# Kernel tuning notes

Measured on AMD Instinct MI355X. Metric: run time of the kernel, lower is better.

The kernel has to match this reference:

```python
import jax, jax.numpy as jnp
import numpy as np

B, N, E, F, H = 4, 10000, 320000, 128, 128


def setup_inputs() -> dict:
    key = jax.random.key(0)
    ks = jax.random.split(key, 12)
    s = 1.0 / np.sqrt(F)
    sh = 1.0 / np.sqrt(H)
    return {
        "batch_feat": jax.random.normal(ks[0], (B, N, F), dtype=jnp.float32),
        "batch_edges": jax.random.randint(ks[1], (B, 2, E), 0, N, dtype=jnp.int32),
        "batch_attr": jax.random.uniform(ks[2], (B, E), dtype=jnp.float32),
        "W1": jax.random.uniform(ks[3], (F, H), jnp.float32, -s, s),
        "b1": jnp.zeros((H,), jnp.float32),
        "W2": jax.random.uniform(ks[4], (H, H), jnp.float32, -sh, sh),
        "b2": jnp.zeros((H,), jnp.float32),
        "W3": jax.random.uniform(ks[5], (H, H), jnp.float32, -sh, sh),
        "b3": jnp.zeros((H,), jnp.float32),
        "Wl": jax.random.uniform(ks[6], (H, 1), jnp.float32, -sh, sh),
        "bl": jnp.zeros((1,), jnp.float32),
    }


def reference(batch_feat, batch_edges, batch_attr, W1, b1, W2, b2, W3, b3, Wl, bl):
    n_nodes = batch_feat.shape[1]

    def gcn_conv(x, row, col, w, W, b):
        # PyG gcn_norm with add_self_loops=False: deg = scatter_add(w, col)
        deg = jax.ops.segment_sum(w, col, num_segments=n_nodes)  # [N]
        dinv = jnp.where(deg > 0, jax.lax.rsqrt(deg), 0.0)
        norm = dinv[row] * w * dinv[col]                         # [E]
        xw = x @ W                                               # [N,H]
        msg = norm[:, None] * xw[row]                            # gather [E,H]
        return jax.ops.segment_sum(msg, col, num_segments=n_nodes) + b

    def per_graph(x, ei, w):
        row, col = ei[0], ei[1]
        h = jax.nn.relu(gcn_conv(x, row, col, w, W1, b1))
        h = jax.nn.relu(gcn_conv(h, row, col, w, W2, b2))
        h = jax.nn.relu(gcn_conv(h, row, col, w, W3, b3))
        return h.mean(axis=0) @ Wl + bl                          # [1]

    return jax.vmap(per_graph)(batch_feat, batch_edges, batch_attr)  # [B,1]
```

## Files before the change

### kernel.cpp

```cpp
#include <hip/hip_runtime.h>

#define BB 4
#define NN 10000
#define EE 320000
#define HH 128
#define HALFN 5000
#define NK2 (2 * NN)
#define RS (2 * NN + 1)

__global__ __launch_bounds__(256) void rank_kernel(
    const int* __restrict__ edges, int* __restrict__ cnt, int* __restrict__ rank) {
  int b = blockIdx.y;
  int e0 = (blockIdx.x * 256 + threadIdx.x) * 2;
  int2 rr = *(const int2*)(edges + (size_t)b * 2 * EE + e0);
  int2 cc = *(const int2*)(edges + (size_t)b * 2 * EE + EE + e0);
  int k0 = ((rr.x >= HALFN) ? NN : 0) + cc.x;
  int k1 = ((rr.y >= HALFN) ? NN : 0) + cc.y;
  int r0 = atomicAdd(&cnt[b * NK2 + k0], 1);
  int r1 = atomicAdd(&cnt[b * NK2 + k1], 1);
  *(int2*)(rank + (size_t)b * EE + e0) = make_int2(r0, r1);
}

__global__ __launch_bounds__(256) void scan_kernel(
    const int* __restrict__ cnt, int* __restrict__ rowstart) {
  int b = blockIdx.x, t = threadIdx.x;
  __shared__ int s[256];
  int running = 0;
  for (int base = 0; base < NK2; base += 2048) {
    int v[8];
    int i0 = base + t * 8;
    int tsum = 0;
#pragma unroll
    for (int j = 0; j < 8; ++j) {
      v[j] = (i0 + j < NK2) ? cnt[b * NK2 + i0 + j] : 0;
      tsum += v[j];
    }
    s[t] = tsum;
    __syncthreads();
    for (int o = 1; o < 256; o <<= 1) {
      int add = (t >= o) ? s[t - o] : 0;
      __syncthreads();
      s[t] += add;
      __syncthreads();
    }
    int ex = running + s[t] - tsum;
#pragma unroll
    for (int j = 0; j < 8; ++j) {
      if (i0 + j < NK2) rowstart[b * RS + i0 + j] = ex;
      ex += v[j];
    }
    int tot = s[255];
    __syncthreads();
    running += tot;
  }
  if (t == 0) rowstart[b * RS + NK2] = running;
}

__global__ __launch_bounds__(256) void fill_kernel(
    const int* __restrict__ edges, const float* __restrict__ attr,
    const int* __restrict__ rank, const int* __restrict__ rowstart,
    int2* __restrict__ csr) {
  int b = blockIdx.y;
  int e0 = (blockIdx.x * 256 + threadIdx.x) * 2;
  int2 rr = *(const int2*)(edges + (size_t)b * 2 * EE + e0);
  int2 cc = *(const int2*)(edges + (size_t)b * 2 * EE + EE + e0);
  float2 ww = *(const float2*)(attr + (size_t)b * EE + e0);
  int2 rk = *(const int2*)(rank + (size_t)b * EE + e0);
  int k0 = ((rr.x >= HALFN) ? NN : 0) + cc.x;
  int k1 = ((rr.y >= HALFN) ? NN : 0) + cc.y;
  int p0 = rowstart[b * RS + k0] + rk.x;
  int p1 = rowstart[b * RS + k1] + rk.y;
  csr[(size_t)b * EE + p0] = make_int2(rr.x, __float_as_int(ww.x));
  csr[(size_t)b * EE + p1] = make_int2(rr.y, __float_as_int(ww.y));
}

__global__ __launch_bounds__(256) void deg_kernel(
    const int2* __restrict__ csr, const int* __restrict__ rowstart,
    float* __restrict__ dinv) {
  int b = blockIdx.y;
  int n = blockIdx.x * 256 + threadIdx.x;
  if (n >= NN) return;
  const int2* c = csr + (size_t)b * EE;
  float sum = 0.f;
#pragma unroll
  for (int q = 0; q < 2; ++q) {
    int key = q * NN + n;
    int s0 = rowstart[b * RS + key], s1 = rowstart[b * RS + key + 1];
    for (int i = s0; i < s1; ++i) sum += __int_as_float(c[i].y);
  }
  dinv[b * NN + n] = sum > 0.f ? rsqrtf(sum) : 0.f;
}

__global__ __launch_bounds__(256) void gemm_kernel(
    const float* __restrict__ x, const float* __restrict__ W,
    float* __restrict__ out) {
  __shared__ float xs[32 * 68];
  __shared__ float ws[32 * 144];
  int b = blockIdx.y;
  int row0 = blockIdx.x * 64;
  int t = threadIdx.x;
  int rg = t >> 4, cg = t & 15;
  int fc = cg * 8 + ((cg >> 2) << 2);
  float acc[4][8];
#pragma unroll
  for (int r = 0; r < 4; ++r)
#pragma unroll
    for (int j = 0; j < 8; ++j) acc[r][j] = 0.f;
  const float* xb = x + (size_t)b * NN * HH;

  for (int k0 = 0; k0 < HH; k0 += 32) {
#pragma unroll
    for (int i = 0; i < 2; ++i) {
      int idx = t + i * 256;
      int rl = idx >> 3, kq = idx & 7;
      int row = row0 + rl;
      float4 v = make_float4(0.f, 0.f, 0.f, 0.f);
      if (row < NN) v = *(const float4*)(xb + (size_t)row * HH + k0 + kq * 4);
      xs[(kq * 4 + 0) * 68 + rl] = v.x;
      xs[(kq * 4 + 1) * 68 + rl] = v.y;
      xs[(kq * 4 + 2) * 68 + rl] = v.z;
      xs[(kq * 4 + 3) * 68 + rl] = v.w;
    }
#pragma unroll
    for (int i = 0; i < 4; ++i) {
      int idx = t + i * 256;
      int kk = idx >> 5, c = (idx & 31) * 4;
      float4 v = *(const float4*)(W + (size_t)(k0 + kk) * HH + c);
      int f = c + ((c >> 5) << 2);
      *(float4*)&ws[kk * 144 + f] = v;
    }
    __syncthreads();
#pragma unroll 4
    for (int k = 0; k < 32; ++k) {
      float4 xv = *(const float4*)&xs[k * 68 + rg * 4];
      float4 w0 = *(const float4*)&ws[k * 144 + fc];
      float4 w1 = *(const float4*)&ws[k * 144 + fc + 4];
      const float* xp = (const float*)&xv;
#pragma unroll
      for (int r = 0; r < 4; ++r) {
        acc[r][0] += xp[r] * w0.x; acc[r][1] += xp[r] * w0.y;
        acc[r][2] += xp[r] * w0.z; acc[r][3] += xp[r] * w0.w;
        acc[r][4] += xp[r] * w1.x; acc[r][5] += xp[r] * w1.y;
        acc[r][6] += xp[r] * w1.z; acc[r][7] += xp[r] * w1.w;
      }
    }
    __syncthreads();
  }
#pragma unroll
  for (int r = 0; r < 4; ++r) {
    int row = row0 + rg * 4 + r;
    if (row < NN) {
      float* og = out + ((size_t)b * NN + row) * HH + cg * 8;
      *(float4*)og = make_float4(acc[r][0], acc[r][1], acc[r][2], acc[r][3]);
      *(float4*)(og + 4) = make_float4(acc[r][4], acc[r][5], acc[r][6], acc[r][7]);
    }
  }
}

__global__ __launch_bounds__(256) void agg_kernel(
    const float* __restrict__ xw, const int2* __restrict__ csr,
    const int* __restrict__ rowstart, const float* __restrict__ dinv,
    const float* __restrict__ bias, float* __restrict__ h, int phase) {
  int g = blockIdx.x & 7;
  int b = g >> 1;
  int q = g & 1;
  int chunk = blockIdx.x >> 3;
  int nhalf = (phase == 0) ? q : 1 - q;
  int half = (threadIdx.x >> 5) & 1;
  int n = nhalf * HALFN + chunk * 8 + (threadIdx.x >> 6) * 2 + half;
  int sl = threadIdx.x & 31;
  int key = q * NN + n;
  int s0 = rowstart[b * RS + key], s1 = rowstart[b * RS + key + 1];
  const float* xwg = xw + (size_t)b * NN * HH;
  const float* dv = dinv + b * NN;
  const int2* c = csr + (size_t)b * EE;
  float4 a0 = make_float4(0.f, 0.f, 0.f, 0.f);
  float4 a1 = make_float4(0.f, 0.f, 0.f, 0.f);
  float4 a2 = make_float4(0.f, 0.f, 0.f, 0.f);
  float4 a3 = make_float4(0.f, 0.f, 0.f, 0.f);
  int i = s0;
  for (; i + 4 <= s1; i += 4) {
    int2 e0 = c[i];
    int2 e1 = c[i + 1];
    int2 e2 = c[i + 2];
    int2 e3 = c[i + 3];
    float w0 = __int_as_float(e0.y) * dv[e0.x];
    float w1 = __int_as_float(e1.y) * dv[e1.x];
    float w2 = __int_as_float(e2.y) * dv[e2.x];
    float w3 = __int_as_float(e3.y) * dv[e3.x];
    float4 v0 = *(const float4*)(xwg + (size_t)e0.x * HH + sl * 4);
    float4 v1 = *(const float4*)(xwg + (size_t)e1.x * HH + sl * 4);
    float4 v2 = *(const float4*)(xwg + (size_t)e2.x * HH + sl * 4);
    float4 v3 = *(const float4*)(xwg + (size_t)e3.x * HH + sl * 4);
    a0.x += w0 * v0.x; a0.y += w0 * v0.y; a0.z += w0 * v0.z; a0.w += w0 * v0.w;
    a1.x += w1 * v1.x; a1.y += w1 * v1.y; a1.z += w1 * v1.z; a1.w += w1 * v1.w;
    a2.x += w2 * v2.x; a2.y += w2 * v2.y; a2.z += w2 * v2.z; a2.w += w2 * v2.w;
    a3.x += w3 * v3.x; a3.y += w3 * v3.y; a3.z += w3 * v3.z; a3.w += w3 * v3.w;
  }
  for (; i < s1; ++i) {
    int2 e0 = c[i];
    float w0 = __int_as_float(e0.y) * dv[e0.x];
    float4 v0 = *(const float4*)(xwg + (size_t)e0.x * HH + sl * 4);
    a0.x += w0 * v0.x; a0.y += w0 * v0.y; a0.z += w0 * v0.z; a0.w += w0 * v0.w;
  }
  a0.x += a1.x + a2.x + a3.x;
  a0.y += a1.y + a2.y + a3.y;
  a0.z += a1.z + a2.z + a3.z;
  a0.w += a1.w + a2.w + a3.w;
  float* hp = h + ((size_t)b * NN + n) * HH + sl * 4;
  if (phase == 0) {
    *(float4*)hp = a0;
  } else {
    float dn = dv[n];
    float4 prev = *(const float4*)hp;
    float4 bb = *(const float4*)(bias + sl * 4);
    *(float4*)hp = make_float4(fmaxf((prev.x + a0.x) * dn + bb.x, 0.f),
                               fmaxf((prev.y + a0.y) * dn + bb.y, 0.f),
                               fmaxf((prev.z + a0.z) * dn + bb.z, 0.f),
                               fmaxf((prev.w + a0.w) * dn + bb.w, 0.f));
  }
}

__global__ __launch_bounds__(64) void init_out_kernel(float* out, const float* __restrict__ bl) {
  if (threadIdx.x < BB) out[threadIdx.x] = bl[0];
}

__global__ __launch_bounds__(256) void final_kernel(
    const float* __restrict__ h, const float* __restrict__ Wl,
    float* __restrict__ out) {
  int b = blockIdx.y;
  int t = threadIdx.x;
  int f = t & 127;
  int rr = t >> 7;
  float p = 0.f;
  for (int n = blockIdx.x * 2 + rr; n < NN; n += gridDim.x * 2)
    p += h[((size_t)b * NN + n) * HH + f];
  __shared__ float s[256];
  s[t] = p;
  __syncthreads();
  float v = 0.f;
  if (t < 128) v = (s[t] + s[t + 128]) * Wl[f];
  __syncthreads();
  s[t] = v;
  __syncthreads();
  for (int o = 64; o > 0; o >>= 1) {
    if (t < o) s[t] += s[t + o];
    __syncthreads();
  }
  if (t == 0) atomicAdd(&out[b], s[0] * (1.0f / NN));
}

extern "C" void kernel_launch(void* const* d_in, const int* in_sizes, int n_in,
                              void* d_out, int out_size, void* d_ws, size_t ws_size,
                              hipStream_t stream) {
  const float* feat = (const float*)d_in[0];
  const int* edges = (const int*)d_in[1];
  const float* attr = (const float*)d_in[2];
  const float* W1 = (const float*)d_in[3];
  const float* b1 = (const float*)d_in[4];
  const float* W2 = (const float*)d_in[5];
  const float* b2 = (const float*)d_in[6];
  const float* W3 = (const float*)d_in[7];
  const float* b3 = (const float*)d_in[8];
  const float* Wl = (const float*)d_in[9];
  const float* bl = (const float*)d_in[10];
  float* out = (float*)d_out;

  char* ws = (char*)d_ws;
  size_t off = 0;
  auto alloc = [&](size_t bytes) {
    size_t o = off;
    off = (off + bytes + 255) & ~(size_t)255;
    return o;
  };
  int*   cnt      = (int*)  (ws + alloc((size_t)BB * NK2 * 4));
  int*   rowstart = (int*)  (ws + alloc((size_t)BB * RS * 4));
  int2*  csr      = (int2*) (ws + alloc((size_t)BB * EE * 8));
  float* xw       = (float*)(ws + alloc((size_t)BB * NN * HH * 4));
  float* h        = (float*)(ws + alloc((size_t)BB * NN * HH * 4));
  int*   rank = (int*)xw;
  float* dinv = (float*)cnt;

  (void)hipMemsetAsync(cnt, 0, (size_t)BB * NK2 * 4, stream);

  dim3 egrid2(EE / 512, BB);
  rank_kernel<<<egrid2, 256, 0, stream>>>(edges, cnt, rank);
  scan_kernel<<<BB, 256, 0, stream>>>(cnt, rowstart);
  fill_kernel<<<egrid2, 256, 0, stream>>>(edges, attr, rank, rowstart, csr);
  deg_kernel<<<dim3((NN + 255) / 256, BB), 256, 0, stream>>>(csr, rowstart, dinv);

  dim3 ggrid((NN + 63) / 64, BB);
  int agrid = 8 * (HALFN / 8);

  gemm_kernel<<<ggrid, 256, 0, stream>>>(feat, W1, xw);
  agg_kernel<<<agrid, 256, 0, stream>>>(xw, csr, rowstart, dinv, b1, h, 0);
  agg_kernel<<<agrid, 256, 0, stream>>>(xw, csr, rowstart, dinv, b1, h, 1);
  gemm_kernel<<<ggrid, 256, 0, stream>>>(h, W2, xw);
  agg_kernel<<<agrid, 256, 0, stream>>>(xw, csr, rowstart, dinv, b2, h, 0);
  agg_kernel<<<agrid, 256, 0, stream>>>(xw, csr, rowstart, dinv, b2, h, 1);
  gemm_kernel<<<ggrid, 256, 0, stream>>>(h, W3, xw);
  agg_kernel<<<agrid, 256, 0, stream>>>(xw, csr, rowstart, dinv, b3, h, 0);
  agg_kernel<<<agrid, 256, 0, stream>>>(xw, csr, rowstart, dinv, b3, h, 1);

  init_out_kernel<<<1, 64, 0, stream>>>(out, bl);
  final_kernel<<<dim3(64, BB), 256, 0, stream>>>(h, Wl, out);
}
```

Measured before the change: 381.9 us.

## Replace global atomic ranking with per-block LDS histograms and column scan

Swaps the global-atomic counting sort used to build the CSR for a two-level scheme. Each of 64 blocks per graph builds a shared-memory histogram of destination columns, one half of the row split at a time, and records 16-bit local ranks. A column-scan kernel then turns the per-block histograms into block offsets and totals, and the fill kernel adds the global rowstart, the block offset and the local rank. This removes heavily contended global atomics, but adds a 64x20000 histogram buffer written and scanned per graph, an extra launch, and blocks that run only 256 threads with a 40 KB LDS array.

Result: faster. 373.3 us (-2.2%).

```diff
diff --git a/kernel.cpp b/kernel.cpp
--- a/kernel.cpp
+++ b/kernel.cpp
@@ -7,18 +7,51 @@
 #define HALFN 5000
 #define NK2 (2 * NN)
 #define RS (2 * NN + 1)
-
-__global__ __launch_bounds__(256) void rank_kernel(
-    const int* __restrict__ edges, int* __restrict__ cnt, int* __restrict__ rank) {
-  int b = blockIdx.y;
-  int e0 = (blockIdx.x * 256 + threadIdx.x) * 2;
-  int2 rr = *(const int2*)(edges + (size_t)b * 2 * EE + e0);
-  int2 cc = *(const int2*)(edges + (size_t)b * 2 * EE + EE + e0);
-  int k0 = ((rr.x >= HALFN) ? NN : 0) + cc.x;
-  int k1 = ((rr.y >= HALFN) ? NN : 0) + cc.y;
-  int r0 = atomicAdd(&cnt[b * NK2 + k0], 1);
-  int r1 = atomicAdd(&cnt[b * NK2 + k1], 1);
-  *(int2*)(rank + (size_t)b * EE + e0) = make_int2(r0, r1);
+#define NHB 64
+#define EPB (EE / NHB)
+
+__global__ __launch_bounds__(256) void hist_kernel(
+    const int* __restrict__ edges, int* __restrict__ hb,
+    unsigned short* __restrict__ lrank) {
+  __shared__ int lh[NN];
+  int b = blockIdx.y;
+  int blk = blockIdx.x;
+  int t = threadIdx.x;
+  const int* rows = edges + (size_t)b * 2 * EE;
+  const int* cols = rows + EE;
+#pragma unroll
+  for (int half = 0; half < 2; ++half) {
+    for (int i = t; i < NN; i += 256) lh[i] = 0;
+    __syncthreads();
+    for (int i = t; i < EPB; i += 256) {
+      int e = blk * EPB + i;
+      int row = rows[e];
+      int col = cols[e];
+      if ((row >= HALFN) == (half != 0)) {
+        int lr = atomicAdd(&lh[col], 1);
+        lrank[(size_t)b * EE + e] = (unsigned short)lr;
+      }
+    }
+    __syncthreads();
+    int* hbrow = hb + ((size_t)(b * NHB + blk)) * NK2 + half * NN;
+    for (int i = t; i < NN; i += 256) hbrow[i] = lh[i];
+    __syncthreads();
+  }
+}
+
+__global__ __launch_bounds__(256) void colscan_kernel(
+    int* __restrict__ hb, int* __restrict__ cnt) {
+  int b = blockIdx.y;
+  int k = blockIdx.x * 256 + threadIdx.x;
+  if (k >= NK2) return;
+  int acc = 0;
+  for (int j = 0; j < NHB; ++j) {
+    size_t idx = ((size_t)(b * NHB + j)) * NK2 + k;
+    int v = hb[idx];
+    hb[idx] = acc;
+    acc += v;
+  }
+  cnt[b * NK2 + k] = acc;
 }
 
 __global__ __launch_bounds__(256) void scan_kernel(
@@ -58,18 +91,20 @@
 
 __global__ __launch_bounds__(256) void fill_kernel(
     const int* __restrict__ edges, const float* __restrict__ attr,
-    const int* __restrict__ rank, const int* __restrict__ rowstart,
-    int2* __restrict__ csr) {
+    const unsigned short* __restrict__ lrank, const int* __restrict__ hb,
+    const int* __restrict__ rowstart, int2* __restrict__ csr) {
   int b = blockIdx.y;
   int e0 = (blockIdx.x * 256 + threadIdx.x) * 2;
+  int blk = e0 / EPB;
   int2 rr = *(const int2*)(edges + (size_t)b * 2 * EE + e0);
   int2 cc = *(const int2*)(edges + (size_t)b * 2 * EE + EE + e0);
   float2 ww = *(const float2*)(attr + (size_t)b * EE + e0);
-  int2 rk = *(const int2*)(rank + (size_t)b * EE + e0);
+  unsigned int lr2 = *(const unsigned int*)(lrank + (size_t)b * EE + e0);
   int k0 = ((rr.x >= HALFN) ? NN : 0) + cc.x;
   int k1 = ((rr.y >= HALFN) ? NN : 0) + cc.y;
-  int p0 = rowstart[b * RS + k0] + rk.x;
-  int p1 = rowstart[b * RS + k1] + rk.y;
+  const int* hbrow = hb + ((size_t)(b * NHB + blk)) * NK2;
+  int p0 = rowstart[b * RS + k0] + hbrow[k0] + (int)(lr2 & 0xffffu);
+  int p1 = rowstart[b * RS + k1] + hbrow[k1] + (int)(lr2 >> 16);
   csr[(size_t)b * EE + p0] = make_int2(rr.x, __float_as_int(ww.x));
   csr[(size_t)b * EE + p1] = make_int2(rr.y, __float_as_int(ww.y));
 }
@@ -278,15 +313,16 @@
   int2*  csr      = (int2*) (ws + alloc((size_t)BB * EE * 8));
   float* xw       = (float*)(ws + alloc((size_t)BB * NN * HH * 4));
   float* h        = (float*)(ws + alloc((size_t)BB * NN * HH * 4));
-  int*   rank = (int*)xw;
+  unsigned short* lrank = (unsigned short*)xw;
+  int*   hb   = (int*)h;
   float* dinv = (float*)cnt;
 
-  (void)hipMemsetAsync(cnt, 0, (size_t)BB * NK2 * 4, stream);
-
+  dim3 hgrid(NHB, BB);
+  hist_kernel<<<hgrid, 256, 0, stream>>>(edges, hb, lrank);
+  colscan_kernel<<<dim3((NK2 + 255) / 256, BB), 256, 0, stream>>>(hb, cnt);
+  scan_kernel<<<BB, 256, 0, stream>>>(cnt, rowstart);
   dim3 egrid2(EE / 512, BB);
-  rank_kernel<<<egrid2, 256, 0, stream>>>(edges, cnt, rank);
-  scan_kernel<<<BB, 256, 0, stream>>>(cnt, rowstart);
-  fill_kernel<<<egrid2, 256, 0, stream>>>(edges, attr, rank, rowstart, csr);
+  fill_kernel<<<egrid2, 256, 0, stream>>>(edges, attr, lrank, hb, rowstart, csr);
   deg_kernel<<<dim3((NN + 255) / 256, BB), 256, 0, stream>>>(csr, rowstart, dinv);
 
   dim3 ggrid((NN + 63) / 64, BB);
```
